# Kernel optimization log

Measured on AMD Instinct MI355X. Metric: run time of the kernel, lower is better.

Reference implementation:

```python
import jax, jax.numpy as jnp
import numpy as np

B, S, H, NH, HD, I, W = 2, 4096, 1024, 16, 64, 4096, 512
EPS = 1e-6


def rotate_every_two(x):
    # x: (..., HD) -> interleave (-x2, x1)
    x2 = x.reshape(x.shape[:-1] + (HD // 2, 2))
    r = jnp.stack((-x2[..., 1], x2[..., 0]), axis=-1)
    return r.reshape(x.shape)


def apply_rope(x, sin, cos):
    # x: (B,S,NH,HD); sin/cos: (S,1,HD) -> (1,S,1,HD)
    sin = sin[None]
    cos = cos[None]
    return x * cos + rotate_every_two(x) * sin


def local_attention(q, k, v, width):
    # q,k,v: (B,S,NH,HD); causal windowed attention: j <= i and i-j < width
    nb = S // width
    scale = 1.0 / np.sqrt(HD)

    def blk(t):  # (B,S,NH,HD) -> (B,NH,nb,W,HD)
        return t.reshape(B, nb, width, NH, HD).transpose(0, 3, 1, 2, 4)

    qb, kb, vb = blk(q), blk(k), blk(v)
    zpad = jnp.zeros((B, NH, 1, width, HD), dtype=q.dtype)
    kp = jnp.concatenate([zpad, kb], axis=2)
    vp = jnp.concatenate([zpad, vb], axis=2)
    # keys/values for block n: [block n-1, block n] -> (B,NH,nb,2W,HD)
    keys = jnp.concatenate([kp[:, :, :-1], kp[:, :, 1:]], axis=3)
    vals = jnp.concatenate([vp[:, :, :-1], vp[:, :, 1:]], axis=3)

    scores = jnp.einsum('bhnqd,bhnkd->bhnqk', qb, keys) * scale

    qi = jnp.arange(width)[:, None]            # (W,1)
    ki = jnp.arange(2 * width)[None, :]        # (1,2W)
    rel = qi - (ki - width)                    # i - j within a block
    nidx = jnp.arange(nb)[:, None, None]
    jglob = nidx * width + (ki - width)[None]  # global key index
    mask = (rel >= 0) & (rel < width) & (jglob >= 0)  # (nb,W,2W)

    neg = jnp.asarray(jnp.finfo(scores.dtype).min, scores.dtype)
    scores = jnp.where(mask[None, None], scores, neg)
    p = jax.nn.softmax(scores, axis=-1)
    out = jnp.einsum('bhnqk,bhnkd->bhnqd', p, vals)  # (B,NH,nb,W,HD)
    return out.transpose(0, 2, 3, 1, 4).reshape(B, S, NH, HD)


def setup_inputs() -> dict:
    key = jax.random.key(0)
    ks = jax.random.split(key, 8)
    x = jax.random.normal(ks[0], (B, S, H), dtype=jnp.float32)
    # rotary sin/cos, interleaved-pair convention matching rotate_every_two
    inv_freq = 1.0 / (10000.0 ** (np.arange(0, HD, 2) / HD))  # (HD/2,)
    ang = np.arange(S)[:, None] * inv_freq[None, :]           # (S, HD/2)
    sin = jnp.asarray(np.repeat(np.sin(ang), 2, axis=-1), jnp.float32)[:, None, :]
    cos = jnp.asarray(np.repeat(np.cos(ang), 2, axis=-1), jnp.float32)[:, None, :]
    norm_w = jnp.ones((H,), jnp.float32)
    w_qkv = jax.random.normal(ks[1], (H, 3 * H), jnp.float32) * 0.02
    b_qkv = jnp.zeros((3 * H,), jnp.float32)
    w_in = jax.random.normal(ks[2], (H, I), jnp.float32) * 0.02
    b_in = jnp.zeros((I,), jnp.float32)
    w_out = jax.random.normal(ks[3], (H + I, H), jnp.float32) * 0.02
    b_out = jnp.zeros((H,), jnp.float32)
    return {"x": x, "sin": sin, "cos": cos, "norm_w": norm_w,
            "w_qkv": w_qkv, "b_qkv": b_qkv, "w_in": w_in, "b_in": b_in,
            "w_out": w_out, "b_out": b_out, "attention_width": W}


def reference(x, sin, cos, norm_w, w_qkv, b_qkv, w_in, b_in, w_out, b_out, attention_width):
    # RMSNorm
    xn = x * jax.lax.rsqrt(jnp.mean(x * x, axis=-1, keepdims=True) + EPS) * norm_w
    # fused QKV
    qkv = (xn @ w_qkv + b_qkv).reshape(B, S, 3, NH, HD)
    q = apply_rope(qkv[:, :, 0], sin, cos)
    k = apply_rope(qkv[:, :, 1], sin, cos)
    v = qkv[:, :, 2]
    attn = local_attention(q, k, v, attention_width).reshape(B, S, H)
    # parallel FFN branch
    ff = jax.nn.gelu(xn @ w_in + b_in, approximate=False)
    combined = jnp.concatenate([attn, ff], axis=-1)
    return combined @ w_out + b_out
```

## Files before the change

### kernel.cpp

```cpp
#include <hip/hip_runtime.h>

typedef unsigned short u16;
typedef __attribute__((ext_vector_type(8))) short short8;
typedef __attribute__((ext_vector_type(4))) unsigned short u16x4;
typedef __attribute__((ext_vector_type(4))) float f32x4;

#define DEV __device__ __forceinline__
#define VMW(n) asm volatile("s_waitcnt vmcnt(" #n ")" ::: "memory")

DEV float bf2f(u16 u) { return __uint_as_float(((unsigned int)u) << 16); }
DEV u16 f2bf(float f) {
  unsigned int u = __float_as_uint(f);
  u += 0x7FFF + ((u >> 16) & 1);
  return (u16)(u >> 16);
}

DEV float redmax16(float v) {
  v = fmaxf(v, __shfl_xor(v, 1));
  v = fmaxf(v, __shfl_xor(v, 2));
  v = fmaxf(v, __shfl_xor(v, 4));
  v = fmaxf(v, __shfl_xor(v, 8));
  return v;
}
DEV float redsum16(float v) {
  v += __shfl_xor(v, 1);
  v += __shfl_xor(v, 2);
  v += __shfl_xor(v, 4);
  v += __shfl_xor(v, 8);
  return v;
}

__global__ __launch_bounds__(256) void transpose_f32_bf16(const float* __restrict__ in,
                                                          u16* __restrict__ out,
                                                          int R, int C) {
  __shared__ u16 tile[32][33];
  int tx = threadIdx.x & 31, ty = threadIdx.x >> 5;
  int r0 = blockIdx.y * 32, c0 = blockIdx.x * 32;
#pragma unroll
  for (int i = 0; i < 32; i += 8)
    tile[ty + i][tx] = f2bf(in[(size_t)(r0 + ty + i) * C + c0 + tx]);
  __syncthreads();
#pragma unroll
  for (int i = 0; i < 32; i += 8)
    out[(size_t)(c0 + ty + i) * R + r0 + tx] = tile[tx][ty + i];
}

__global__ __launch_bounds__(256) void rmsnorm_kernel(const float* __restrict__ x,
                                                      const float* __restrict__ w,
                                                      u16* __restrict__ xn) {
  int row = blockIdx.x, t = threadIdx.x;
  const float4* xr = reinterpret_cast<const float4*>(x + (size_t)row * 1024);
  float4 v = xr[t];
  float ss = v.x * v.x + v.y * v.y + v.z * v.z + v.w * v.w;
#pragma unroll
  for (int d = 1; d < 64; d <<= 1) ss += __shfl_xor(ss, d);
  __shared__ float red[4];
  if ((t & 63) == 0) red[t >> 6] = ss;
  __syncthreads();
  float tot = red[0] + red[1] + red[2] + red[3];
  float inv = rsqrtf(tot * (1.0f / 1024.0f) + 1e-6f);
  float4 wv = reinterpret_cast<const float4*>(w)[t];
  u16x4 o;
  o[0] = f2bf(v.x * inv * wv.x);
  o[1] = f2bf(v.y * inv * wv.y);
  o[2] = f2bf(v.z * inv * wv.z);
  o[3] = f2bf(v.w * inv * wv.w);
  *reinterpret_cast<u16x4*>(xn + (size_t)row * 1024 + t * 4) = o;
}

DEV void stage_half(const u16* __restrict__ gbase, int K, int kt, char* dst, int w, int l) {
#pragma unroll
  for (int j = 0; j < 2; ++j) {
    int s = w * 2 + j;
    int row = s * 8 + (l >> 3);
    int ksrc = ((l & 7) ^ (l >> 3)) << 3;
    const u16* src = gbase + (size_t)row * K + kt + ksrc;
    __builtin_amdgcn_global_load_lds(
        (const __attribute__((address_space(1))) unsigned int*)src,
        (__attribute__((address_space(3))) unsigned int*)(dst + s * 1024 + l * 16),
        16, 0, 0);
  }
}

DEV short8 ldfrag(const char* base, int row, int slot) {
  return *reinterpret_cast<const short8*>(base + row * 128 + (((slot ^ (row & 7)) << 4)));
}

__global__ __launch_bounds__(512) void gemm256(const u16* __restrict__ A,
                                               const u16* __restrict__ BT,
                                               const float* __restrict__ bias,
                                               void* __restrict__ Cout,
                                               u16* __restrict__ vTout,
                                               const float* __restrict__ sp,
                                               const float* __restrict__ cp,
                                               int K, int ldc, int mode) {
  __shared__ float4 lds_v[9216];
  char* lds = (char*)lds_v;
  int t = threadIdx.x;
  int w = t >> 6, l = t & 63, c = l & 15, g = l >> 4;
  int wr = w >> 1, wc = w & 1;
  size_t m0 = (size_t)blockIdx.y * 256, n0 = (size_t)blockIdx.x * 128;
  const u16* Ab = A + m0 * K;
  const u16* Bb = BT + n0 * K;
  int KT = K >> 6;

  f32x4 zero4 = {0.f, 0.f, 0.f, 0.f};
  f32x4 acc[4][4];
#pragma unroll
  for (int a = 0; a < 4; ++a)
#pragma unroll
    for (int b2 = 0; b2 < 4; ++b2) acc[a][b2] = zero4;

#pragma unroll
  for (int pt = 0; pt < 2; ++pt) {
    int boff = pt * 49152;
    stage_half(Ab, K, pt * 64, lds + boff, w, l);
    stage_half(Ab + (size_t)128 * K, K, pt * 64, lds + boff + 16384, w, l);
    stage_half(Bb, K, pt * 64, lds + boff + 32768, w, l);
  }
  VMW(6);
  __builtin_amdgcn_s_barrier();

  for (int tt = 0; tt < KT; ++tt) {
    const char* Abuf = lds + (tt % 3) * 49152;
    const char* Bbuf = Abuf + 32768;
    int b2off = ((tt + 2) % 3) * 49152;
    int kt2 = (tt + 2) * 64;
    bool pf = (tt + 2 < KT);

    if (pf) {
      stage_half(Ab, K, kt2, lds + b2off, w, l);
      stage_half(Ab + (size_t)128 * K, K, kt2, lds + b2off + 16384, w, l);
    }
    {
      short8 bv[4], av[4];
#pragma unroll
      for (int nj = 0; nj < 4; ++nj) bv[nj] = ldfrag(Bbuf, wc * 64 + 16 * nj + c, g);
#pragma unroll
      for (int mi = 0; mi < 4; ++mi) av[mi] = ldfrag(Abuf, wr * 64 + 16 * mi + c, g);
      __builtin_amdgcn_s_setprio(1);
#pragma unroll
      for (int mi = 0; mi < 4; ++mi)
#pragma unroll
        for (int nj = 0; nj < 4; ++nj)
          acc[mi][nj] = __builtin_amdgcn_mfma_f32_16x16x32_bf16(av[mi], bv[nj], acc[mi][nj], 0, 0, 0);
      __builtin_amdgcn_s_setprio(0);
    }
    __builtin_amdgcn_s_barrier();

    if (pf) stage_half(Bb, K, kt2, lds + b2off + 32768, w, l);
    {
      short8 bv[4], av[4];
#pragma unroll
      for (int nj = 0; nj < 4; ++nj) bv[nj] = ldfrag(Bbuf, wc * 64 + 16 * nj + c, 4 + g);
#pragma unroll
      for (int mi = 0; mi < 4; ++mi) av[mi] = ldfrag(Abuf, wr * 64 + 16 * mi + c, 4 + g);
      __builtin_amdgcn_s_setprio(1);
#pragma unroll
      for (int mi = 0; mi < 4; ++mi)
#pragma unroll
        for (int nj = 0; nj < 4; ++nj)
          acc[mi][nj] = __builtin_amdgcn_mfma_f32_16x16x32_bf16(av[mi], bv[nj], acc[mi][nj], 0, 0, 0);
      __builtin_amdgcn_s_setprio(0);
    }
    if (tt + 1 < KT) {
      if (pf)
        VMW(6);
      else
        VMW(0);
      __builtin_amdgcn_s_barrier();
    }
  }

  if (mode == 3) {
    bool blockV = (n0 >= 2048);
    if (!blockV) {
#pragma unroll
      for (int nj = 0; nj < 4; ++nj) {
        int col = (int)n0 + wc * 64 + 16 * nj + c;
        float bvv = bias[col];
        float sgn = (col & 1) ? 1.0f : -1.0f;
        float scq = (col < 1024) ? 0.125f : 1.0f;
        int d = col & 63;
#pragma unroll
        for (int mi = 0; mi < 4; ++mi) {
          size_t rbase = m0 + wr * 64 + 16 * mi + 4 * g;
#pragma unroll
          for (int r = 0; r < 4; ++r) {
            float fb = acc[mi][nj][r] + bvv;
            float fp = __shfl_xor(fb, 1);
            int pos = (int)((rbase + r) & 4095);
            float sv = sp[pos * 64 + d];
            float cv = cp[pos * 64 + d];
            ((u16*)Cout)[(rbase + r) * (size_t)ldc + col] = f2bf((fb * cv + sgn * fp * sv) * scq);
          }
        }
      }
    } else {
      int b16 = ((int)(m0 >> 12)) * 16;
#pragma unroll
      for (int nj = 0; nj < 4; ++nj) {
        int col = (int)n0 + wc * 64 + 16 * nj + c;
        float bvv = bias[col];
        int cv2 = col - 2048;
        int h = cv2 >> 6, d = cv2 & 63;
        u16* vb = vTout + ((size_t)(b16 + h)) * 262144 + (size_t)d * 4096;
#pragma unroll
        for (int mi = 0; mi < 4; ++mi) {
          size_t rbase = m0 + wr * 64 + 16 * mi + 4 * g;
          int s0 = (int)(rbase & 4095);
          u16x4 pk;
#pragma unroll
          for (int r = 0; r < 4; ++r) pk[r] = f2bf(acc[mi][nj][r] + bvv);
          *reinterpret_cast<u16x4*>(vb + s0) = pk;
        }
      }
    }
    return;
  }

#pragma unroll
  for (int nj = 0; nj < 4; ++nj) {
    int col = (int)n0 + wc * 64 + 16 * nj + c;
    float bvv = bias[col];
#pragma unroll
    for (int mi = 0; mi < 4; ++mi) {
      size_t rbase = m0 + wr * 64 + 16 * mi + 4 * g;
#pragma unroll
      for (int r = 0; r < 4; ++r) {
        float f = acc[mi][nj][r] + bvv;
        if (mode == 1) f = 0.5f * f * (1.0f + erff(f * 0.70710678f));
        size_t oidx = (rbase + r) * (size_t)ldc + col;
        if (mode == 2)
          ((float*)Cout)[oidx] = f;
        else
          ((u16*)Cout)[oidx] = f2bf(f);
      }
    }
  }
}

__global__ __launch_bounds__(64) void attn_kernel(const u16* __restrict__ qk,
                                                  const u16* __restrict__ vT,
                                                  u16* __restrict__ comb) {
  int bid = blockIdx.x;
  int swz = ((bid & 7) << 9) + (bid >> 3);
  int qt = swz & 127, h = (swz >> 7) & 15, b = swz >> 11;
  int l = threadIdx.x, c = l & 15, g = l >> 4;
  int q0 = qt * 32;
  const u16* qb = qk + (size_t)b * 4096 * 2048 + h * 64;
  const u16* kb = qb + 1024;
  const u16* vt = vT + (size_t)(b * 16 + h) * 64 * 4096;
  __shared__ u16 Pl[32 * 72];

  short8 qf[2][2];
#pragma unroll
  for (int mi = 0; mi < 2; ++mi)
#pragma unroll
    for (int kk = 0; kk < 2; ++kk)
      qf[mi][kk] = *reinterpret_cast<const short8*>(
          qb + (size_t)(q0 + 16 * mi + c) * 2048 + 32 * kk + 8 * g);

  f32x4 zero4 = {0.f, 0.f, 0.f, 0.f};
  f32x4 o[2][4];
  float mr[2][4], lr[2][4];
#pragma unroll
  for (int a = 0; a < 2; ++a)
#pragma unroll
    for (int d2 = 0; d2 < 4; ++d2) {
      o[a][d2] = zero4;
      mr[a][d2] = -1e30f;
      lr[a][d2] = 0.f;
    }

  int t_lo = (q0 >= 480) ? ((q0 - 480) >> 6) : 0;
  int t_hi = (q0 + 31) >> 6;

  short8 kfc[2][4], kfn[2][4], bv[2][4];
#pragma unroll
  for (int kk = 0; kk < 2; ++kk)
#pragma unroll
    for (int nj = 0; nj < 4; ++nj)
      kfc[kk][nj] = *reinterpret_cast<const short8*>(
          kb + (size_t)(t_lo * 64 + 16 * nj + c) * 2048 + 32 * kk + 8 * g);

  for (int tt = t_lo; tt <= t_hi; ++tt) {
    int kt0 = tt * 64;

#pragma unroll
    for (int kk = 0; kk < 2; ++kk)
#pragma unroll
      for (int dj = 0; dj < 4; ++dj)
        bv[kk][dj] = *reinterpret_cast<const short8*>(
            vt + (size_t)(16 * dj + c) * 4096 + kt0 + 32 * kk + 8 * g);

    if (tt < t_hi) {
#pragma unroll
      for (int kk = 0; kk < 2; ++kk)
#pragma unroll
        for (int nj = 0; nj < 4; ++nj)
          kfn[kk][nj] = *reinterpret_cast<const short8*>(
              kb + (size_t)(kt0 + 64 + 16 * nj + c) * 2048 + 32 * kk + 8 * g);
    }

    f32x4 s[2][4];
#pragma unroll
    for (int a = 0; a < 2; ++a)
#pragma unroll
      for (int d2 = 0; d2 < 4; ++d2) s[a][d2] = zero4;
#pragma unroll
    for (int kk = 0; kk < 2; ++kk)
#pragma unroll
      for (int mi = 0; mi < 2; ++mi)
#pragma unroll
        for (int nj = 0; nj < 4; ++nj)
          s[mi][nj] = __builtin_amdgcn_mfma_f32_16x16x32_bf16(qf[mi][kk], kfc[kk][nj], s[mi][nj], 0, 0, 0);

    bool mc = (tt == t_hi), mw = (tt == t_lo);
    if (mc | mw) {
#pragma unroll
      for (int mi = 0; mi < 2; ++mi)
#pragma unroll
        for (int nj = 0; nj < 4; ++nj)
#pragma unroll
          for (int r = 0; r < 4; ++r) {
            int qg = q0 + 16 * mi + 4 * g + r;
            int kg = kt0 + 16 * nj + c;
            if ((mc && kg > qg) || (mw && qg - kg >= 512)) s[mi][nj][r] = -1e30f;
          }
    }

#pragma unroll
    for (int mi = 0; mi < 2; ++mi)
#pragma unroll
      for (int r = 0; r < 4; ++r) {
        float tm = fmaxf(fmaxf(s[mi][0][r], s[mi][1][r]), fmaxf(s[mi][2][r], s[mi][3][r]));
        tm = redmax16(tm);
        float mn = fmaxf(mr[mi][r], tm);
        float a = __expf(mr[mi][r] - mn);
        mr[mi][r] = mn;
        float rs = 0.f;
        u16* pp = &Pl[(16 * mi + 4 * g + r) * 72 + c];
#pragma unroll
        for (int nj = 0; nj < 4; ++nj) {
          float p = __expf(s[mi][nj][r] - mn);
          rs += p;
          pp[16 * nj] = f2bf(p);
        }
        rs = redsum16(rs);
        lr[mi][r] = lr[mi][r] * a + rs;
#pragma unroll
        for (int dj = 0; dj < 4; ++dj) o[mi][dj][r] *= a;
      }

#pragma unroll
    for (int kk = 0; kk < 2; ++kk) {
      short8 pa[2];
#pragma unroll
      for (int mi = 0; mi < 2; ++mi)
        pa[mi] = *reinterpret_cast<const short8*>(&Pl[(16 * mi + c) * 72 + 32 * kk + 8 * g]);
#pragma unroll
      for (int mi = 0; mi < 2; ++mi)
#pragma unroll
        for (int dj = 0; dj < 4; ++dj)
          o[mi][dj] = __builtin_amdgcn_mfma_f32_16x16x32_bf16(pa[mi], bv[kk][dj], o[mi][dj], 0, 0, 0);
    }

    if (tt < t_hi) {
#pragma unroll
      for (int kk = 0; kk < 2; ++kk)
#pragma unroll
        for (int nj = 0; nj < 4; ++nj) kfc[kk][nj] = kfn[kk][nj];
    }
  }

  u16* ob = comb + (size_t)(b * 4096 + q0) * 5120 + h * 64;
#pragma unroll
  for (int mi = 0; mi < 2; ++mi)
#pragma unroll
    for (int r = 0; r < 4; ++r) {
      float inv = __builtin_amdgcn_rcpf(lr[mi][r]);
#pragma unroll
      for (int dj = 0; dj < 4; ++dj)
        ob[(size_t)(16 * mi + 4 * g + r) * 5120 + 16 * dj + c] = f2bf(o[mi][dj][r] * inv);
    }
}

extern "C" void kernel_launch(void* const* d_in, const int* in_sizes, int n_in,
                              void* d_out, int out_size, void* d_ws, size_t ws_size,
                              hipStream_t stream) {
  const float* x = (const float*)d_in[0];
  const float* sinp = (const float*)d_in[1];
  const float* cosp = (const float*)d_in[2];
  const float* norm_w = (const float*)d_in[3];
  const float* w_qkv = (const float*)d_in[4];
  const float* b_qkv = (const float*)d_in[5];
  const float* w_in = (const float*)d_in[6];
  const float* b_in = (const float*)d_in[7];
  const float* w_out = (const float*)d_in[8];
  const float* b_out = (const float*)d_in[9];
  float* out = (float*)d_out;

  char* ws = (char*)d_ws;
  u16* xn = (u16*)(ws);
  u16* qk = (u16*)(ws + 16777216);
  u16* vT = (u16*)(ws + 50331648);
  u16* comb = (u16*)(ws + 67108864);
  u16* wqkvT = (u16*)(ws + 150994944);
  u16* winT = (u16*)(ws + 157286400);
  u16* woutT = (u16*)(ws + 165675008);

  transpose_f32_bf16<<<dim3(3072 / 32, 1024 / 32), 256, 0, stream>>>(w_qkv, wqkvT, 1024, 3072);
  transpose_f32_bf16<<<dim3(4096 / 32, 1024 / 32), 256, 0, stream>>>(w_in, winT, 1024, 4096);
  transpose_f32_bf16<<<dim3(1024 / 32, 5120 / 32), 256, 0, stream>>>(w_out, woutT, 5120, 1024);

  rmsnorm_kernel<<<8192, 256, 0, stream>>>(x, norm_w, xn);

  gemm256<<<dim3(3072 / 128, 8192 / 256), 512, 0, stream>>>(
      xn, wqkvT, b_qkv, qk, vT, sinp, cosp, 1024, 2048, 3);

  gemm256<<<dim3(4096 / 128, 8192 / 256), 512, 0, stream>>>(
      xn, winT, b_in, comb + 1024, nullptr, nullptr, nullptr, 1024, 5120, 1);

  attn_kernel<<<4096, 64, 0, stream>>>(qk, vT, comb);

  gemm256<<<dim3(1024 / 128, 8192 / 256), 512, 0, stream>>>(
      comb, woutT, b_out, out, nullptr, nullptr, nullptr, 5120, 1024, 2);
}
```

Measured before the change: 391.8 us.

## Merge weight transposes into one launch and add lazy softmax rescaling

```diff
diff --git a/kernel.cpp b/kernel.cpp
--- a/kernel.cpp
+++ b/kernel.cpp
@@ -30,12 +30,31 @@
   return v;
 }
 
-__global__ __launch_bounds__(256) void transpose_f32_bf16(const float* __restrict__ in,
-                                                          u16* __restrict__ out,
-                                                          int R, int C) {
+__global__ __launch_bounds__(256) void transpose_all(const float* __restrict__ w_qkv,
+                                                     const float* __restrict__ w_in,
+                                                     const float* __restrict__ w_out,
+                                                     u16* __restrict__ wqkvT,
+                                                     u16* __restrict__ winT,
+                                                     u16* __restrict__ woutT) {
   __shared__ u16 tile[32][33];
+  int bid = blockIdx.x;
+  const float* in;
+  u16* out;
+  int R, C, bx, by;
+  if (bid < 3072) {
+    in = w_qkv; out = wqkvT; R = 1024; C = 3072;
+    bx = bid % 96; by = bid / 96;
+  } else if (bid < 7168) {
+    int b = bid - 3072;
+    in = w_in; out = winT; R = 1024; C = 4096;
+    bx = b % 128; by = b / 128;
+  } else {
+    int b = bid - 7168;
+    in = w_out; out = woutT; R = 5120; C = 1024;
+    bx = b % 32; by = b / 32;
+  }
   int tx = threadIdx.x & 31, ty = threadIdx.x >> 5;
-  int r0 = blockIdx.y * 32, c0 = blockIdx.x * 32;
+  int r0 = by * 32, c0 = bx * 32;
 #pragma unroll
   for (int i = 0; i < 32; i += 8)
     tile[ty + i][tx] = f2bf(in[(size_t)(r0 + ty + i) * C + c0 + tx]);
@@ -330,27 +349,45 @@
           }
     }
 
+    float tmv[2][4];
+    float dmax = -1e30f;
 #pragma unroll
     for (int mi = 0; mi < 2; ++mi)
 #pragma unroll
       for (int r = 0; r < 4; ++r) {
         float tm = fmaxf(fmaxf(s[mi][0][r], s[mi][1][r]), fmaxf(s[mi][2][r], s[mi][3][r]));
         tm = redmax16(tm);
-        float mn = fmaxf(mr[mi][r], tm);
-        float a = __expf(mr[mi][r] - mn);
-        mr[mi][r] = mn;
+        tmv[mi][r] = tm;
+        dmax = fmaxf(dmax, tm - mr[mi][r]);
+      }
+    if (!__all(dmax <= 8.0f)) {
+#pragma unroll
+      for (int mi = 0; mi < 2; ++mi)
+#pragma unroll
+        for (int r = 0; r < 4; ++r) {
+          float mn = fmaxf(mr[mi][r], tmv[mi][r]);
+          float a = __expf(mr[mi][r] - mn);
+          mr[mi][r] = mn;
+          lr[mi][r] *= a;
+#pragma unroll
+          for (int dj = 0; dj < 4; ++dj) o[mi][dj][r] *= a;
+        }
+    }
+
+#pragma unroll
+    for (int mi = 0; mi < 2; ++mi)
+#pragma unroll
+      for (int r = 0; r < 4; ++r) {
         float rs = 0.f;
         u16* pp = &Pl[(16 * mi + 4 * g + r) * 72 + c];
 #pragma unroll
         for (int nj = 0; nj < 4; ++nj) {
-          float p = __expf(s[mi][nj][r] - mn);
+          float p = __expf(s[mi][nj][r] - mr[mi][r]);
           rs += p;
           pp[16 * nj] = f2bf(p);
         }
         rs = redsum16(rs);
-        lr[mi][r] = lr[mi][r] * a + rs;
-#pragma unroll
-        for (int dj = 0; dj < 4; ++dj) o[mi][dj][r] *= a;
+        lr[mi][r] += rs;
       }
 
 #pragma unroll
@@ -410,9 +447,7 @@
   u16* winT = (u16*)(ws + 157286400);
   u16* woutT = (u16*)(ws + 165675008);
 
-  transpose_f32_bf16<<<dim3(3072 / 32, 1024 / 32), 256, 0, stream>>>(w_qkv, wqkvT, 1024, 3072);
-  transpose_f32_bf16<<<dim3(4096 / 32, 1024 / 32), 256, 0, stream>>>(w_in, winT, 1024, 4096);
-  transpose_f32_bf16<<<dim3(1024 / 32, 5120 / 32), 256, 0, stream>>>(w_out, woutT, 5120, 1024);
+  transpose_all<<<12288, 256, 0, stream>>>(w_qkv, w_in, w_out, wqkvT, winT, woutT);
 
   rmsnorm_kernel<<<8192, 256, 0, stream>>>(x, norm_w, xn);
 
```

After: 382.2 us. -2.5%, faster.
